# Optimization experiments

Hardware: AMD Instinct MI355X
Metric: run time of the kernel (lower is better)

## Reference

```python
import jax, jax.numpy as jnp
import numpy as np

B, HW, ENC, DEC, ATTN = 512, 196, 2048, 512, 512

def setup_inputs() -> dict:
    key = jax.random.key(0)
    ks = jax.random.split(key, 8)
    s_enc = 1.0 / np.sqrt(ENC)
    s_dec = 1.0 / np.sqrt(DEC)
    s_v = 1.0 / np.sqrt(ATTN)
    return {
        "enc_out": jax.random.normal(ks[0], (B, HW, ENC), dtype=jnp.float32),
        "dec_h": jax.random.normal(ks[1], (B, DEC), dtype=jnp.float32),
        "W_enc": jax.random.uniform(ks[2], (ENC, ATTN), jnp.float32, -s_enc, s_enc),
        "b_enc": jax.random.uniform(ks[3], (ATTN,), jnp.float32, -s_enc, s_enc),
        "W_dec": jax.random.uniform(ks[4], (DEC, ATTN), jnp.float32, -s_dec, s_dec),
        "b_dec": jax.random.uniform(ks[5], (ATTN,), jnp.float32, -s_dec, s_dec),
        "W_v": jax.random.uniform(ks[6], (ATTN,), jnp.float32, -s_v, s_v),
        "b_v": jax.random.uniform(ks[7], (), jnp.float32, -s_v, s_v),
    }

def reference(enc_out, dec_h, W_enc, b_enc, W_dec, b_dec, W_v, b_v):
    # attn1: [B, HW, ATTN]; attn2: [B, 1, ATTN]
    attn1 = jnp.einsum('bse,ea->bsa', enc_out, W_enc) + b_enc
    attn2 = (dec_h @ W_dec + b_dec)[:, None, :]
    score = jax.nn.relu(attn1 + attn2)
    logits = jnp.einsum('bsa,a->bs', score, W_v) + b_v  # [B, HW]
    alpha = jax.nn.softmax(logits, axis=1)
    context_vec = jnp.einsum('bs,bse->be', alpha, enc_out)
    return (context_vec, alpha)
```

## Files before the change

kernel.cpp:

```cpp
#include <hip/hip_runtime.h>
#include <hip/hip_bf16.h>
#include <cstdint>
#include <cstddef>

#define B_    512
#define HW_   196
#define ENC_  2048
#define DEC_  512
#define ATTN_ 512
#define M_    (B_*HW_)

typedef __attribute__((ext_vector_type(8))) short short8;
typedef __attribute__((ext_vector_type(4))) float f32x4;

__device__ __forceinline__ unsigned short f2bf(float x) {
  __bf16 b = (__bf16)x;
  return __builtin_bit_cast(unsigned short, b);
}
__device__ __forceinline__ unsigned int cvt2(float x, float y) {
  return (unsigned)f2bf(x) | ((unsigned)f2bf(y) << 16);
}

__device__ __forceinline__ void gload_lds16(const void* g, void* l) {
  __builtin_amdgcn_global_load_lds(
      (const __attribute__((address_space(1))) void*)g,
      (__attribute__((address_space(3))) void*)l, 16, 0, 0);
}

__device__ __forceinline__ int invswz8(int p) {
  const int b2 = ((p >> 2) ^ (p >> 4)) & 1;
  const int b1 = ((p >> 1) ^ (p >> 3)) & 1;
  const int b0 = (p ^ (p >> 2) ^ (p >> 4)) & 1;
  return (p & ~7) | (b2 << 2) | (b1 << 1) | b0;
}

__global__ __launch_bounds__(256)
void k_convert(const float* __restrict__ in, unsigned short* __restrict__ out) {
  const size_t total  = (size_t)M_ * ENC_;
  const size_t stride = (size_t)gridDim.x * 256 * 8;
  for (size_t i = ((size_t)blockIdx.x * 256 + threadIdx.x) * 8; i < total; i += stride) {
    const float4 a = *reinterpret_cast<const float4*>(in + i);
    const float4 b = *reinterpret_cast<const float4*>(in + i + 4);
    uint4 o;
    o.x = cvt2(a.x, a.y);  o.y = cvt2(a.z, a.w);
    o.z = cvt2(b.x, b.y);  o.w = cvt2(b.z, b.w);
    *reinterpret_cast<uint4*>(out + i) = o;
  }
}

__global__ __launch_bounds__(256)
void k_attn2(const float* __restrict__ dec_h, const float* __restrict__ Wdec,
             const float* __restrict__ bdec, const float* __restrict__ benc,
             float* __restrict__ attn2p) {
  __shared__ float dh[DEC_];
  const int b = blockIdx.x;
  const int t = threadIdx.x;
  dh[t]       = dec_h[b*DEC_ + t];
  dh[t + 256] = dec_h[b*DEC_ + t + 256];
  __syncthreads();
  #pragma unroll
  for (int rep = 0; rep < 2; ++rep) {
    const int a = t + rep*256;
    float acc = bdec[a] + benc[a];
    #pragma unroll 8
    for (int k = 0; k < DEC_; ++k)
      acc = fmaf(dh[k], Wdec[(size_t)k*ATTN_ + a], acc);
    attn2p[(size_t)b*ATTN_ + a] = acc;
  }
}

__global__ __launch_bounds__(256)
void k_transpose(const float* __restrict__ Wenc, unsigned short* __restrict__ WencT) {
  __shared__ float tile[32][33];
  const int e0 = blockIdx.x * 32;
  const int a0 = blockIdx.y * 32;
  const int t  = threadIdx.x;
  const int li = t >> 5;
  const int lj = t & 31;
  #pragma unroll
  for (int rep = 0; rep < 4; ++rep) {
    const int i = li + rep*8;
    tile[i][lj] = Wenc[(size_t)(e0 + i)*ATTN_ + a0 + lj];
  }
  __syncthreads();
  #pragma unroll
  for (int rep = 0; rep < 4; ++rep) {
    const int ar = li + rep*8;
    WencT[(size_t)(a0 + ar)*ENC_ + e0 + lj] = f2bf(tile[lj][ar]);
  }
}

#define BM 128
#define BN 128
#define BK 32
#define NT (ENC_/BK)

__global__ __launch_bounds__(256)
void k_gemm_logits_bf16(const unsigned short* __restrict__ ench,
                        const unsigned short* __restrict__ WencT,
                        const float* __restrict__ attn2p,
                        const float* __restrict__ Wv,
                        float* __restrict__ partials) {
  __shared__ unsigned short As[2][BM*BK];
  __shared__ unsigned short Bs[2][BN*BK];
  __shared__ float plog[BM][2];

  const int tid  = threadIdx.x;
  const int id   = blockIdx.x;
  const int xcd  = id & 7;
  const int rest = id >> 3;
  const int nb   = rest & 3;
  const int mblk = (rest >> 2) * 8 + xcd;
  const int r0 = mblk * BM;
  const int n0 = nb * BN;

  const int w  = tid >> 6;
  const int l  = tid & 63;
  const int wm = w >> 1, wn = w & 1;
  const int lrow = l & 15;
  const int kg   = l >> 4;
  const int g4   = kg << 2;

  int pp[2];
  const unsigned short* aSrc[2];
  const unsigned short* bSrc[2];
  #pragma unroll
  for (int r = 0; r < 2; ++r) {
    const int p = r*256 + tid;
    const int c = invswz8(p);
    const int row = c >> 2, cj = c & 3;
    pp[r]   = p;
    aSrc[r] = ench  + (size_t)(r0 + row)*ENC_ + (size_t)(cj << 3);
    bSrc[r] = WencT + (size_t)(n0 + row)*ENC_ + (size_t)(cj << 3);
  }

  int aOff[4], bOff[4];
  #pragma unroll
  for (int mi = 0; mi < 4; ++mi) {
    const int cr = ((wm*64 + mi*16 + lrow) << 2) + kg;
    aOff[mi] = (cr ^ ((cr >> 2) & 7)) << 3;
  }
  #pragma unroll
  for (int ni = 0; ni < 4; ++ni) {
    const int cr = ((wn*64 + ni*16 + lrow) << 2) + kg;
    bOff[ni] = (cr ^ ((cr >> 2) & 7)) << 3;
  }

  f32x4 acc[4][4];
  #pragma unroll
  for (int mi = 0; mi < 4; ++mi)
    #pragma unroll
    for (int ni = 0; ni < 4; ++ni)
      acc[mi][ni] = (f32x4){0.f, 0.f, 0.f, 0.f};

  #pragma unroll
  for (int r = 0; r < 2; ++r) {
    gload_lds16(aSrc[r], &As[0][pp[r] << 3]);
    gload_lds16(bSrc[r], &Bs[0][pp[r] << 3]);
    aSrc[r] += BK;  bSrc[r] += BK;
  }
  __syncthreads();

#define STEP(P, COND) do {                                                     \
    if (COND) {                                                                \
      _Pragma("unroll")                                                        \
      for (int r = 0; r < 2; ++r) {                                            \
        gload_lds16(aSrc[r], &As[(P)^1][pp[r] << 3]);                          \
        gload_lds16(bSrc[r], &Bs[(P)^1][pp[r] << 3]);                          \
        aSrc[r] += BK;  bSrc[r] += BK;                                         \
      }                                                                        \
    }                                                                          \
    short8 aF[4], bF[4];                                                       \
    _Pragma("unroll")                                                          \
    for (int mi = 0; mi < 4; ++mi)                                             \
      aF[mi] = *reinterpret_cast<const short8*>(&As[P][aOff[mi]]);             \
    _Pragma("unroll")                                                          \
    for (int ni = 0; ni < 4; ++ni)                                             \
      bF[ni] = *reinterpret_cast<const short8*>(&Bs[P][bOff[ni]]);             \
    _Pragma("unroll")                                                          \
    for (int mi = 0; mi < 4; ++mi)                                             \
      _Pragma("unroll")                                                        \
      for (int ni = 0; ni < 4; ++ni)                                           \
        acc[mi][ni] = __builtin_amdgcn_mfma_f32_16x16x32_bf16(                 \
            aF[mi], bF[ni], acc[mi][ni], 0, 0, 0);                             \
    __syncthreads();                                                           \
  } while (0)

  for (int kt = 0; kt < NT; kt += 2) {
    STEP(0, true);
    STEP(1, kt + 2 < NT);
  }
#undef STEP

  float wvv[4];
  #pragma unroll
  for (int ni = 0; ni < 4; ++ni) wvv[ni] = Wv[n0 + wn*64 + ni*16 + lrow];
  #pragma unroll
  for (int mi = 0; mi < 4; ++mi) {
    #pragma unroll
    for (int j = 0; j < 4; ++j) {
      const int row_local = wm*64 + mi*16 + g4 + j;
      const int r  = r0 + row_local;
      const int bb = r / HW_;
      const float* a2 = attn2p + (size_t)bb*ATTN_ + n0 + wn*64;
      float s = 0.f;
      #pragma unroll
      for (int ni = 0; ni < 4; ++ni) {
        float v = acc[mi][ni][j] + a2[ni*16 + lrow];
        v = fmaxf(v, 0.f);
        s = fmaf(v, wvv[ni], s);
      }
      s += __shfl_xor(s, 1);
      s += __shfl_xor(s, 2);
      s += __shfl_xor(s, 4);
      s += __shfl_xor(s, 8);
      if (lrow == 0) plog[row_local][wn] = s;
    }
  }
  __syncthreads();
  if (tid < BM)
    partials[(size_t)(r0 + tid)*4 + nb] = plog[tid][0] + plog[tid][1];
}

#define LDA 40
__global__ __launch_bounds__(256)
void k_gemm_logits_f32(const float* __restrict__ enc,
                       const unsigned short* __restrict__ WencT,
                       const float* __restrict__ attn2p,
                       const float* __restrict__ Wv,
                       float* __restrict__ partials) {
  __shared__ unsigned short As[BM*LDA];
  __shared__ unsigned short Bs[2][BN*BK];
  __shared__ float plog[BM][2];

  const int tid  = threadIdx.x;
  const int id   = blockIdx.x;
  const int xcd  = id & 7;
  const int rest = id >> 3;
  const int nb   = rest & 3;
  const int mblk = (rest >> 2) * 8 + xcd;
  const int r0 = mblk * BM;
  const int n0 = nb * BN;

  const int arow  = tid >> 1;
  const int ahalf = (tid & 1) << 4;
  const float* aptr = enc + (size_t)(r0 + arow)*ENC_ + ahalf;
  const unsigned short* bbase = WencT + (size_t)n0*ENC_;

  const int w  = tid >> 6;
  const int l  = tid & 63;
  const int wm = w >> 1, wn = w & 1;
  const int lrow = l & 15;
  const int kg   = l >> 4;
  const int lk8  = kg << 3;
  const int g4   = kg << 2;

  f32x4 acc[4][4];
  #pragma unroll
  for (int mi = 0; mi < 4; ++mi)
    #pragma unroll
    for (int ni = 0; ni < 4; ++ni)
      acc[mi][ni] = (f32x4){0.f, 0.f, 0.f, 0.f};

  float4 ar[4];
  #pragma unroll
  for (int i = 0; i < 4; ++i) ar[i] = *reinterpret_cast<const float4*>(aptr + i*4);
  #pragma unroll
  for (int r = 0; r < 2; ++r) {
    const int p = r*256 + tid;
    const int c = invswz8(p);
    gload_lds16(bbase + (size_t)(c >> 2)*ENC_ + (c & 3)*8, &Bs[0][p*8]);
  }

  for (int kt = 0; kt < NT; ++kt) {
    {
      unsigned int pk[8];
      #pragma unroll
      for (int i = 0; i < 4; ++i) {
        pk[2*i]   = cvt2(ar[i].x, ar[i].y);
        pk[2*i+1] = cvt2(ar[i].z, ar[i].w);
      }
      uint4* da = reinterpret_cast<uint4*>(&As[arow*LDA + ahalf]);
      da[0] = make_uint4(pk[0], pk[1], pk[2], pk[3]);
      da[1] = make_uint4(pk[4], pk[5], pk[6], pk[7]);
    }
    __syncthreads();
    if (kt + 1 < NT) {
      const float* ap = aptr + (kt + 1)*BK;
      #pragma unroll
      for (int i = 0; i < 4; ++i) ar[i] = *reinterpret_cast<const float4*>(ap + i*4);
      const int k0n = (kt + 1)*BK;
      unsigned short* bdst = Bs[(kt + 1) & 1];
      #pragma unroll
      for (int r = 0; r < 2; ++r) {
        const int p = r*256 + tid;
        const int c = invswz8(p);
        gload_lds16(bbase + (size_t)(c >> 2)*ENC_ + k0n + (c & 3)*8, &bdst[p*8]);
      }
    }
    const unsigned short* bsc = Bs[kt & 1];
    short8 aF[4], bF[4];
    #pragma unroll
    for (int mi = 0; mi < 4; ++mi)
      aF[mi] = *reinterpret_cast<const short8*>(&As[(wm*64 + mi*16 + lrow)*LDA + lk8]);
    #pragma unroll
    for (int ni = 0; ni < 4; ++ni) {
      const int cr = ((wn*64 + ni*16 + lrow) << 2) + kg;
      const int pr = cr ^ ((cr >> 2) & 7);
      bF[ni] = *reinterpret_cast<const short8*>(&bsc[pr << 3]);
    }
    #pragma unroll
    for (int mi = 0; mi < 4; ++mi)
      #pragma unroll
      for (int ni = 0; ni < 4; ++ni)
        acc[mi][ni] = __builtin_amdgcn_mfma_f32_16x16x32_bf16(aF[mi], bF[ni], acc[mi][ni], 0, 0, 0);
    __syncthreads();
  }

  float wvv[4];
  #pragma unroll
  for (int ni = 0; ni < 4; ++ni) wvv[ni] = Wv[n0 + wn*64 + ni*16 + lrow];
  #pragma unroll
  for (int mi = 0; mi < 4; ++mi) {
    #pragma unroll
    for (int j = 0; j < 4; ++j) {
      const int row_local = wm*64 + mi*16 + g4 + j;
      const int r  = r0 + row_local;
      const int bb = r / HW_;
      const float* a2 = attn2p + (size_t)bb*ATTN_ + n0 + wn*64;
      float s = 0.f;
      #pragma unroll
      for (int ni = 0; ni < 4; ++ni) {
        float v = acc[mi][ni][j] + a2[ni*16 + lrow];
        v = fmaxf(v, 0.f);
        s = fmaf(v, wvv[ni], s);
      }
      s += __shfl_xor(s, 1);
      s += __shfl_xor(s, 2);
      s += __shfl_xor(s, 4);
      s += __shfl_xor(s, 8);
      if (lrow == 0) plog[row_local][wn] = s;
    }
  }
  __syncthreads();
  if (tid < BM)
    partials[(size_t)(r0 + tid)*4 + nb] = plog[tid][0] + plog[tid][1];
}

__global__ __launch_bounds__(64)
void k_softmax(const float* __restrict__ partials, const float* __restrict__ bvp,
               float* __restrict__ alpha) {
  const int b = blockIdx.x;
  const int t = threadIdx.x;
  const float bv = bvp[0];
  float lg[4];
  #pragma unroll
  for (int i = 0; i < 4; ++i) {
    const int s = t + i*64;
    if (s < HW_) {
      const float4 p = *reinterpret_cast<const float4*>(&partials[(size_t)(b*HW_ + s)*4]);
      lg[i] = p.x + p.y + p.z + p.w + bv;
    } else lg[i] = -INFINITY;
  }
  float mx = fmaxf(fmaxf(lg[0], lg[1]), fmaxf(lg[2], lg[3]));
  #pragma unroll
  for (int off = 32; off; off >>= 1) mx = fmaxf(mx, __shfl_xor(mx, off));
  float sum = 0.f;
  #pragma unroll
  for (int i = 0; i < 4; ++i) { lg[i] = expf(lg[i] - mx); sum += lg[i]; }
  #pragma unroll
  for (int off = 32; off; off >>= 1) sum += __shfl_xor(sum, off);
  const float inv = 1.0f / sum;
  #pragma unroll
  for (int i = 0; i < 4; ++i) {
    const int s = t + i*64;
    if (s < HW_) alpha[b*HW_ + s] = lg[i] * inv;
  }
}

__global__ __launch_bounds__(256)
void k_context_bf16(const unsigned short* __restrict__ ench,
                    const float* __restrict__ alpha, float* __restrict__ ctx) {
  __shared__ float al[HW_];
  const int b = blockIdx.x;
  const int t = threadIdx.x;
  if (t < HW_) al[t] = alpha[b*HW_ + t];
  __syncthreads();
  const unsigned short* base = ench + (size_t)b*HW_*ENC_ + t*8;
  float acc[8] = {0.f,0.f,0.f,0.f,0.f,0.f,0.f,0.f};
  #pragma unroll 2
  for (int s = 0; s < HW_; ++s) {
    const uint4 v = *reinterpret_cast<const uint4*>(base + (size_t)s*ENC_);
    const float a = al[s];
    const unsigned u[4] = {v.x, v.y, v.z, v.w};
    #pragma unroll
    for (int q = 0; q < 4; ++q) {
      const float lo = __builtin_bit_cast(float, u[q] << 16);
      const float hi = __builtin_bit_cast(float, u[q] & 0xffff0000u);
      acc[2*q]   = fmaf(a, lo, acc[2*q]);
      acc[2*q+1] = fmaf(a, hi, acc[2*q+1]);
    }
  }
  float4* o = reinterpret_cast<float4*>(&ctx[(size_t)b*ENC_ + t*8]);
  o[0] = make_float4(acc[0], acc[1], acc[2], acc[3]);
  o[1] = make_float4(acc[4], acc[5], acc[6], acc[7]);
}

__global__ __launch_bounds__(256)
void k_context_f32(const float* __restrict__ enc, const float* __restrict__ alpha,
                   float* __restrict__ ctx) {
  __shared__ float al[HW_];
  const int bi = blockIdx.x;
  const int b  = bi >> 1;
  const int e0 = (bi & 1) << 10;
  const int t  = threadIdx.x;
  if (t < HW_) al[t] = alpha[b*HW_ + t];
  __syncthreads();
  const float* base = enc + (size_t)b*HW_*ENC_ + e0 + t*4;
  float4 acc = {0.f, 0.f, 0.f, 0.f};
  #pragma unroll 4
  for (int s = 0; s < HW_; ++s) {
    const float a = al[s];
    const float4 v = *reinterpret_cast<const float4*>(base + (size_t)s*ENC_);
    acc.x = fmaf(a, v.x, acc.x);
    acc.y = fmaf(a, v.y, acc.y);
    acc.z = fmaf(a, v.z, acc.z);
    acc.w = fmaf(a, v.w, acc.w);
  }
  *reinterpret_cast<float4*>(&ctx[(size_t)b*ENC_ + e0 + t*4]) = acc;
}

extern "C" void kernel_launch(void* const* d_in, const int* in_sizes, int n_in,
                              void* d_out, int out_size, void* d_ws, size_t ws_size,
                              hipStream_t stream) {
  const float* enc   = (const float*)d_in[0];
  const float* dec_h = (const float*)d_in[1];
  const float* Wenc  = (const float*)d_in[2];
  const float* benc  = (const float*)d_in[3];
  const float* Wdec  = (const float*)d_in[4];
  const float* bdec  = (const float*)d_in[5];
  const float* Wv    = (const float*)d_in[6];
  const float* bv    = (const float*)d_in[7];

  float* ctx   = (float*)d_out;
  float* alpha = (float*)d_out + (size_t)B_*ENC_;

  char* ws = (char*)d_ws;
  float*          attn2p   = (float*)ws;
  unsigned short* WencT    = (unsigned short*)(ws + (1u << 20));
  float*          partials = (float*)(ws + 3u*(1u << 20));
  unsigned short* ench     = (unsigned short*)(ws + 5u*(1u << 20));
  const size_t needed = 5u*(1u << 20) + (size_t)M_*ENC_*sizeof(unsigned short);
  const bool big = (ws_size >= needed);

  hipLaunchKernelGGL(k_attn2,     dim3(B_),                dim3(256), 0, stream,
                     dec_h, Wdec, bdec, benc, attn2p);
  hipLaunchKernelGGL(k_transpose, dim3(ENC_/32, ATTN_/32), dim3(256), 0, stream,
                     Wenc, WencT);
  if (big) {
    hipLaunchKernelGGL(k_convert,   dim3(2048),            dim3(256), 0, stream,
                       enc, ench);
    hipLaunchKernelGGL(k_gemm_logits_bf16, dim3(3136),     dim3(256), 0, stream,
                       ench, WencT, attn2p, Wv, partials);
    hipLaunchKernelGGL(k_softmax,   dim3(B_),              dim3(64),  0, stream,
                       partials, bv, alpha);
    hipLaunchKernelGGL(k_context_bf16, dim3(B_),           dim3(256), 0, stream,
                       ench, alpha, ctx);
  } else {
    hipLaunchKernelGGL(k_gemm_logits_f32, dim3(3136),      dim3(256), 0, stream,
                       enc, WencT, attn2p, Wv, partials);
    hipLaunchKernelGGL(k_softmax,   dim3(B_),              dim3(64),  0, stream,
                       partials, bv, alpha);
    hipLaunchKernelGGL(k_context_f32, dim3(1024),          dim3(256), 0, stream,
                       enc, alpha, ctx);
  }
}
```

Measured before the change: 803.4 us.

## Replace bf16 logits GEMM with 256x128 tile, 8-wave, triple-buffered pipelined kernel

Replaces the 128x128, 4-wave double-buffered bf16 GEMM with a 256x128 tile kernel using 512 threads, BK=64, and a three-stage LDS ring filled by direct global-to-LDS loads. Explicit vmcnt waits and raw s_barrier calls replace full __syncthreads, and s_setprio raises priority around the MFMA block. The goal is to keep more loads in flight, reuse each B tile across more rows, and overlap memory with compute. In exchange it needs far more LDS, giving one block per CU, and correctness depends on hand-counted waitcnt values.

```diff
diff --git a/kernel.cpp b/kernel.cpp
--- a/kernel.cpp
+++ b/kernel.cpp
@@ -25,13 +25,6 @@
   __builtin_amdgcn_global_load_lds(
       (const __attribute__((address_space(1))) void*)g,
       (__attribute__((address_space(3))) void*)l, 16, 0, 0);
-}
-
-__device__ __forceinline__ int invswz8(int p) {
-  const int b2 = ((p >> 2) ^ (p >> 4)) & 1;
-  const int b1 = ((p >> 1) ^ (p >> 3)) & 1;
-  const int b0 = (p ^ (p >> 2) ^ (p >> 4)) & 1;
-  return (p & ~7) | (b2 << 2) | (b1 << 1) | b0;
 }
 
 __global__ __launch_bounds__(256)
@@ -90,60 +83,60 @@
   }
 }
 
-#define BM 128
-#define BN 128
-#define BK 32
-#define NT (ENC_/BK)
-
-__global__ __launch_bounds__(256)
-void k_gemm_logits_bf16(const unsigned short* __restrict__ ench,
-                        const unsigned short* __restrict__ WencT,
-                        const float* __restrict__ attn2p,
-                        const float* __restrict__ Wv,
-                        float* __restrict__ partials) {
-  __shared__ unsigned short As[2][BM*BK];
-  __shared__ unsigned short Bs[2][BN*BK];
-  __shared__ float plog[BM][2];
-
-  const int tid  = threadIdx.x;
-  const int id   = blockIdx.x;
+#define NKT 32
+
+__global__ __launch_bounds__(512, 1)
+void k_gemm8(const unsigned short* __restrict__ ench,
+             const unsigned short* __restrict__ WencT,
+             const float* __restrict__ attn2p,
+             const float* __restrict__ Wv,
+             float* __restrict__ partials) {
+  __shared__ unsigned short A3[3][256*64];
+  __shared__ unsigned short B3[3][128*64];
+
+  const int tid = threadIdx.x;
+  const int id  = blockIdx.x;
   const int xcd  = id & 7;
   const int rest = id >> 3;
   const int nb   = rest & 3;
-  const int mblk = (rest >> 2) * 8 + xcd;
-  const int r0 = mblk * BM;
-  const int n0 = nb * BN;
+  const int mblk = (rest >> 2)*8 + xcd;
+  const int r0 = mblk * 256;
+  const int n0 = nb * 128;
 
   const int w  = tid >> 6;
   const int l  = tid & 63;
   const int wm = w >> 1, wn = w & 1;
   const int lrow = l & 15;
   const int kg   = l >> 4;
-  const int g4   = kg << 2;
-
-  int pp[2];
-  const unsigned short* aSrc[2];
-  const unsigned short* bSrc[2];
-  #pragma unroll
-  for (int r = 0; r < 2; ++r) {
-    const int p = r*256 + tid;
-    const int c = invswz8(p);
-    const int row = c >> 2, cj = c & 3;
-    pp[r]   = p;
-    aSrc[r] = ench  + (size_t)(r0 + row)*ENC_ + (size_t)(cj << 3);
-    bSrc[r] = WencT + (size_t)(n0 + row)*ENC_ + (size_t)(cj << 3);
-  }
-
-  int aOff[4], bOff[4];
-  #pragma unroll
-  for (int mi = 0; mi < 4; ++mi) {
-    const int cr = ((wm*64 + mi*16 + lrow) << 2) + kg;
-    aOff[mi] = (cr ^ ((cr >> 2) & 7)) << 3;
-  }
-  #pragma unroll
-  for (int ni = 0; ni < 4; ++ni) {
-    const int cr = ((wn*64 + ni*16 + lrow) << 2) + kg;
-    bOff[ni] = (cr ^ ((cr >> 2) & 7)) << 3;
+
+  const unsigned short* aBase[2];
+  #pragma unroll
+  for (int i = 0; i < 2; ++i) {
+    const int j  = tid + i*512;
+    const int rr = j >> 3;
+    const int kc = (j & 7) ^ (rr & 7);
+    aBase[i] = ench + (size_t)(r0 + rr)*ENC_ + kc*8;
+  }
+  const unsigned short* bBase;
+  {
+    const int rr = tid >> 3;
+    const int kc = (tid & 7) ^ (rr & 7);
+    bBase = WencT + (size_t)(n0 + rr)*ENC_ + kc*8;
+  }
+
+  int aOff[2][4], bOff[2][4];
+  #pragma unroll
+  for (int ks = 0; ks < 2; ++ks) {
+    #pragma unroll
+    for (int mi = 0; mi < 4; ++mi) {
+      const int row = wm*64 + mi*16 + lrow;
+      aOff[ks][mi] = (row*8 + ((ks*4 + kg) ^ (row & 7))) * 8;
+    }
+    #pragma unroll
+    for (int ni = 0; ni < 4; ++ni) {
+      const int row = wn*64 + ni*16 + lrow;
+      bOff[ks][ni] = (row*8 + ((ks*4 + kg) ^ (row & 7))) * 8;
+    }
   }
 
   f32x4 acc[4][4];
@@ -153,45 +146,58 @@
     for (int ni = 0; ni < 4; ++ni)
       acc[mi][ni] = (f32x4){0.f, 0.f, 0.f, 0.f};
 
-  #pragma unroll
-  for (int r = 0; r < 2; ++r) {
-    gload_lds16(aSrc[r], &As[0][pp[r] << 3]);
-    gload_lds16(bSrc[r], &Bs[0][pp[r] << 3]);
-    aSrc[r] += BK;  bSrc[r] += BK;
-  }
-  __syncthreads();
-
-#define STEP(P, COND) do {                                                     \
-    if (COND) {                                                                \
-      _Pragma("unroll")                                                        \
-      for (int r = 0; r < 2; ++r) {                                            \
-        gload_lds16(aSrc[r], &As[(P)^1][pp[r] << 3]);                          \
-        gload_lds16(bSrc[r], &Bs[(P)^1][pp[r] << 3]);                          \
-        aSrc[r] += BK;  bSrc[r] += BK;                                         \
-      }                                                                        \
-    }                                                                          \
+#define STAGE(KT, KS) do {                                                     \
+    const size_t _ko = (size_t)(KT)*64;                                        \
+    const int _bw = (KT) % 3;                                                  \
+    gload_lds16(aBase[0] + (size_t)(KS)*(128*ENC_) + _ko,                      \
+                &A3[_bw][(KS)*8192 + tid*8]);                                  \
+    gload_lds16(aBase[1] + (size_t)(KS)*(128*ENC_) + _ko,                      \
+                &A3[_bw][(KS)*8192 + 4096 + tid*8]);                           \
+    gload_lds16(bBase    + (size_t)(KS)*(64*ENC_)  + _ko,                      \
+                &B3[_bw][(KS)*4096 + tid*8]);                                  \
+  } while (0)
+
+  STAGE(0, 0); STAGE(0, 1);
+  STAGE(1, 0); STAGE(1, 1);
+  asm volatile("s_waitcnt vmcnt(6)" ::: "memory");
+  __builtin_amdgcn_s_barrier();
+
+#define PHASE(KS) do {                                                         \
     short8 aF[4], bF[4];                                                       \
     _Pragma("unroll")                                                          \
     for (int mi = 0; mi < 4; ++mi)                                             \
-      aF[mi] = *reinterpret_cast<const short8*>(&As[P][aOff[mi]]);             \
+      aF[mi] = *reinterpret_cast<const short8*>(&aB[aOff[KS][mi]]);            \
     _Pragma("unroll")                                                          \
     for (int ni = 0; ni < 4; ++ni)                                             \
-      bF[ni] = *reinterpret_cast<const short8*>(&Bs[P][bOff[ni]]);             \
+      bF[ni] = *reinterpret_cast<const short8*>(&bB[bOff[KS][ni]]);            \
+    if (doStage) STAGE(kt + 2, KS);                                            \
+    __builtin_amdgcn_s_barrier();                                              \
+    __builtin_amdgcn_s_setprio(1);                                             \
     _Pragma("unroll")                                                          \
     for (int mi = 0; mi < 4; ++mi)                                             \
       _Pragma("unroll")                                                        \
       for (int ni = 0; ni < 4; ++ni)                                           \
         acc[mi][ni] = __builtin_amdgcn_mfma_f32_16x16x32_bf16(                 \
             aF[mi], bF[ni], acc[mi][ni], 0, 0, 0);                             \
-    __syncthreads();                                                           \
+    __builtin_amdgcn_s_setprio(0);                                             \
+    if (KS == 1) {                                                             \
+      if (kt < NKT - 3) { asm volatile("s_waitcnt vmcnt(6)" ::: "memory"); }   \
+      else             { asm volatile("s_waitcnt vmcnt(0)" ::: "memory"); }    \
+    }                                                                          \
+    __builtin_amdgcn_s_barrier();                                              \
   } while (0)
 
-  for (int kt = 0; kt < NT; kt += 2) {
-    STEP(0, true);
-    STEP(1, kt + 2 < NT);
-  }
-#undef STEP
-
+  for (int kt = 0; kt < NKT; ++kt) {
+    const unsigned short* aB = &A3[kt % 3][0];
+    const unsigned short* bB = &B3[kt % 3][0];
+    const bool doStage = (kt + 2 < NKT);
+    PHASE(0);
+    PHASE(1);
+  }
+#undef PHASE
+#undef STAGE
+
+  float* plog = reinterpret_cast<float*>(&A3[0][0]);
   float wvv[4];
   #pragma unroll
   for (int ni = 0; ni < 4; ++ni) wvv[ni] = Wv[n0 + wn*64 + ni*16 + lrow];
@@ -199,7 +205,7 @@
   for (int mi = 0; mi < 4; ++mi) {
     #pragma unroll
     for (int j = 0; j < 4; ++j) {
-      const int row_local = wm*64 + mi*16 + g4 + j;
+      const int row_local = wm*64 + mi*16 + kg*4 + j;
       const int r  = r0 + row_local;
       const int bb = r / HW_;
       const float* a2 = attn2p + (size_t)bb*ATTN_ + n0 + wn*64;
@@ -214,15 +220,25 @@
       s += __shfl_xor(s, 2);
       s += __shfl_xor(s, 4);
       s += __shfl_xor(s, 8);
-      if (lrow == 0) plog[row_local][wn] = s;
-    }
-  }
-  __syncthreads();
-  if (tid < BM)
-    partials[(size_t)(r0 + tid)*4 + nb] = plog[tid][0] + plog[tid][1];
-}
-
+      if (lrow == 0) plog[row_local*2 + wn] = s;
+    }
+  }
+  __syncthreads();
+  if (tid < 256)
+    partials[(size_t)(r0 + tid)*4 + nb] = plog[tid*2] + plog[tid*2 + 1];
+}
+
+#define BM 128
+#define BN 128
+#define BK 32
 #define LDA 40
+#define NT (ENC_/BK)
+__device__ __forceinline__ int invswz8(int p) {
+  const int b2 = ((p >> 2) ^ (p >> 4)) & 1;
+  const int b1 = ((p >> 1) ^ (p >> 3)) & 1;
+  const int b0 = (p ^ (p >> 2) ^ (p >> 4)) & 1;
+  return (p & ~7) | (b2 << 2) | (b1 << 1) | b0;
+}
 __global__ __launch_bounds__(256)
 void k_gemm_logits_f32(const float* __restrict__ enc,
                        const unsigned short* __restrict__ WencT,
@@ -232,7 +248,6 @@
   __shared__ unsigned short As[BM*LDA];
   __shared__ unsigned short Bs[2][BN*BK];
   __shared__ float plog[BM][2];
-
   const int tid  = threadIdx.x;
   const int id   = blockIdx.x;
   const int xcd  = id & 7;
@@ -241,12 +256,10 @@
   const int mblk = (rest >> 2) * 8 + xcd;
   const int r0 = mblk * BM;
   const int n0 = nb * BN;
-
   const int arow  = tid >> 1;
   const int ahalf = (tid & 1) << 4;
   const float* aptr = enc + (size_t)(r0 + arow)*ENC_ + ahalf;
   const unsigned short* bbase = WencT + (size_t)n0*ENC_;
-
   const int w  = tid >> 6;
   const int l  = tid & 63;
   const int wm = w >> 1, wn = w & 1;
@@ -254,14 +267,12 @@
   const int kg   = l >> 4;
   const int lk8  = kg << 3;
   const int g4   = kg << 2;
-
   f32x4 acc[4][4];
   #pragma unroll
   for (int mi = 0; mi < 4; ++mi)
     #pragma unroll
     for (int ni = 0; ni < 4; ++ni)
       acc[mi][ni] = (f32x4){0.f, 0.f, 0.f, 0.f};
-
   float4 ar[4];
   #pragma unroll
   for (int i = 0; i < 4; ++i) ar[i] = *reinterpret_cast<const float4*>(aptr + i*4);
@@ -271,7 +282,6 @@
     const int c = invswz8(p);
     gload_lds16(bbase + (size_t)(c >> 2)*ENC_ + (c & 3)*8, &Bs[0][p*8]);
   }
-
   for (int kt = 0; kt < NT; ++kt) {
     {
       unsigned int pk[8];
@@ -316,7 +326,6 @@
         acc[mi][ni] = __builtin_amdgcn_mfma_f32_16x16x32_bf16(aF[mi], bF[ni], acc[mi][ni], 0, 0, 0);
     __syncthreads();
   }
-
   float wvv[4];
   #pragma unroll
   for (int ni = 0; ni < 4; ++ni) wvv[ni] = Wv[n0 + wn*64 + ni*16 + lrow];
@@ -460,7 +469,7 @@
   if (big) {
     hipLaunchKernelGGL(k_convert,   dim3(2048),            dim3(256), 0, stream,
                        enc, ench);
-    hipLaunchKernelGGL(k_gemm_logits_bf16, dim3(3136),     dim3(256), 0, stream,
+    hipLaunchKernelGGL(k_gemm8,     dim3(1568),            dim3(512), 0, stream,
                        ench, WencT, attn2p, Wv, partials);
     hipLaunchKernelGGL(k_softmax,   dim3(B_),              dim3(64),  0, stream,
                        partials, bv, alpha);
```

Measured after the change: 710.1 us. -11.6%, faster.
